# Kernel optimization log

Measured on AMD Instinct MI355X. Metric: run time of the kernel, lower is better.

## Reference

```python
import jax, jax.numpy as jnp
import numpy as np

V, H, B, T = 32000, 1024, 32, 256  # vocab, rnn_size, batch, seq_length


def setup_inputs() -> dict:
    key = jax.random.key(0)
    ks = jax.random.split(key, 6)
    s = 1.0 / np.sqrt(H)
    return {
        "input_data": jax.random.randint(ks[0], (B, T), 0, V, dtype=jnp.int32),
        "targets": jax.random.randint(ks[1], (B, T), 0, V, dtype=jnp.int32),
        "embedding": jax.random.uniform(ks[2], (V, H), minval=-1.0, maxval=1.0, dtype=jnp.float32),
        "softmax_b": jnp.zeros((V,), jnp.float32),
        "W0": (jax.random.normal(ks[3], (2 * H, 4 * H)) * s).astype(jnp.float32),
        "b0": jnp.zeros((4 * H,), jnp.float32),
        "W1": (jax.random.normal(ks[4], (2 * H, 4 * H)) * s).astype(jnp.float32),
        "b1": jnp.zeros((4 * H,), jnp.float32),
    }


def _lstm_step(x, c, h, W, b):
    # TF LSTMCell: gates i, j, f, o; forget_bias = 1.0
    z = jnp.concatenate([x, h], axis=-1) @ W + b  # [B, 4H]
    i, j, f, o = jnp.split(z, 4, axis=-1)
    c2 = c * jax.nn.sigmoid(f + 1.0) + jax.nn.sigmoid(i) * jnp.tanh(j)
    h2 = jax.nn.sigmoid(o) * jnp.tanh(c2)
    return c2, h2


def reference(input_data, targets, embedding, softmax_b, W0, b0, W1, b1):
    x = embedding[input_data]  # [B, T, H]
    Bb, Hh = x.shape[0], embedding.shape[1]
    zeros = jnp.zeros((Bb, Hh), x.dtype)
    init = ((zeros, zeros), (zeros, zeros))  # ((c0,h0),(c1,h1))

    def step(carry, xt):
        (c0, h0), (c1, h1) = carry
        c0, h0 = _lstm_step(xt, c0, h0, W0, b0)
        c1, h1 = _lstm_step(h0, c1, h1, W1, b1)
        return ((c0, h0), (c1, h1)), h1

    _, outs = jax.lax.scan(step, init, jnp.swapaxes(x, 0, 1))  # [T, B, H]
    output = jnp.swapaxes(outs, 0, 1).reshape(-1, Hh)  # [B*T, H]
    logits = output @ embedding.T + softmax_b  # tied softmax weights, [B*T, V]
    labels = targets.reshape(-1)
    logp = jax.nn.log_softmax(logits)
    loss = -jnp.take_along_axis(logp, labels[:, None], axis=1)[:, 0]
    cost = jnp.sum(loss) / Bb
    return logits, cost
```

## Files before the change

### kernel.cpp

```cpp
#include <hip/hip_runtime.h>
#include <hip/hip_bf16.h>

#define DEV static __device__ __forceinline__

typedef unsigned short u16;
typedef unsigned long long u64;
typedef __attribute__((ext_vector_type(8))) short short8;
typedef __attribute__((ext_vector_type(4))) float f32x4;

constexpr int V = 32000, H = 1024, B = 32, T = 256;
constexpr int BT = B * T;
constexpr int G  = 4 * H;
constexpr int NCH = V / 256;
constexpr int NWG2 = 256;
constexpr int RSTRIDE = 32 * 2048 + 2048;

constexpr size_t SZ_WT    = (size_t)G * 2048 * 2;
constexpr size_t OFF_W0T  = 0;
constexpr size_t OFF_W1T  = OFF_W0T + SZ_WT;
constexpr size_t OFF_EBF  = OFF_W1T + SZ_WT;
constexpr size_t OFF_XBF  = OFF_EBF + (size_t)V * H * 2;
constexpr size_t OFF_XP0  = OFF_XBF + (size_t)BT * H * 2;
constexpr size_t OFF_H1   = OFF_XP0 + (size_t)BT * G * 2;
constexpr size_t OFF_HSEQ = OFF_H1 + (size_t)BT * H * 2;
constexpr size_t SZ_HSEQ  = (size_t)(T + 2) * RSTRIDE * 2;
constexpr size_t OFF_SYNC = OFF_HSEQ + SZ_HSEQ;
constexpr size_t SZ_SYNC  = (size_t)2 * 256 * 128 * 4;
constexpr size_t OFF_PMAX = OFF_SYNC + SZ_SYNC;
constexpr size_t OFF_PSUM = OFF_PMAX + (size_t)BT * NCH * 4;
constexpr size_t OFF_LOSS = OFF_PSUM + (size_t)BT * NCH * 4;

DEV u16 f2bf(float x) {
  union { float f; unsigned int u; } v; v.f = x;
  unsigned int r = v.u + 0x7fffu + ((v.u >> 16) & 1u);
  return (u16)(r >> 16);
}
DEV float bf2f(u16 b) {
  union { unsigned int u; float f; } v; v.u = ((unsigned int)b) << 16;
  return v.f;
}
DEV float sigm(float x) { return 1.f / (1.f + expf(-x)); }

DEV void gload_lds16(const u16* g, u16* l) {
  __builtin_amdgcn_global_load_lds(
      (__attribute__((address_space(1))) void*)g,
      (__attribute__((address_space(3))) void*)l, 16, 0, 0);
}


__global__ void k_transpose_cvt(const float* __restrict__ in, u16* __restrict__ out,
                                int R, int C) {
  __shared__ float tile[32][33];
  int bc = blockIdx.x * 32, br = blockIdx.y * 32;
  int tx = threadIdx.x & 31, ty0 = threadIdx.x >> 5;
#pragma unroll
  for (int i = 0; i < 4; ++i) {
    int ty = ty0 + i * 8;
    tile[ty][tx] = in[(size_t)(br + ty) * C + bc + tx];
  }
  __syncthreads();
#pragma unroll
  for (int i = 0; i < 4; ++i) {
    int ty = ty0 + i * 8;
    out[(size_t)(bc + ty) * R + br + tx] = f2bf(tile[tx][ty]);
  }
}

__global__ void k_cvt_bf16(const float* __restrict__ in, u16* __restrict__ out, int n4) {
  int i = blockIdx.x * blockDim.x + threadIdx.x;
  int stride = gridDim.x * blockDim.x;
  for (; i < n4; i += stride) {
    float4 v = ((const float4*)in)[i];
    ushort4 o;
    o.x = f2bf(v.x); o.y = f2bf(v.y); o.z = f2bf(v.z); o.w = f2bf(v.w);
    ((ushort4*)out)[i] = o;
  }
}

__global__ void k_gather_x(const float* __restrict__ emb, const int* __restrict__ inp,
                           u16* __restrict__ Xbf) {
  int row = blockIdx.x;
  int t = row >> 5, b = row & 31;
  int tok = inp[b * T + t];
  const float4* src = (const float4*)(emb + (size_t)tok * H);
  ushort4* dst = (ushort4*)(Xbf + (size_t)row * H);
  float4 v = src[threadIdx.x];
  ushort4 o;
  o.x = f2bf(v.x); o.y = f2bf(v.y); o.z = f2bf(v.z); o.w = f2bf(v.w);
  dst[threadIdx.x] = o;
}

__global__ void k_zero(unsigned int* __restrict__ p, int nwords) {
  int i = blockIdx.x * blockDim.x + threadIdx.x;
  int stride = gridDim.x * blockDim.x;
  for (; i < nwords; i += stride) p[i] = 0u;
}

template <int CMODE>
__global__ __launch_bounds__(256)
void k_gemm(const u16* __restrict__ A, int lda,
            const u16* __restrict__ Bt, int ldb,
            float* __restrict__ C, int ldc,
            const float* __restrict__ bias, int K) {
  __shared__ alignas(16) u16 ldsA[128 * 32];
  __shared__ alignas(16) u16 ldsB[128 * 32];

  unsigned nwg = gridDim.x * gridDim.y;
  unsigned flat = blockIdx.y * gridDim.x + blockIdx.x;
  unsigned nf = (flat & 7) * (nwg >> 3) + (flat >> 3);
  unsigned bx = nf % gridDim.x, by = nf / gridDim.x;

  int tid = threadIdx.x, lane = tid & 63, w = tid >> 6;
  int row0 = by * 128, col0 = bx * 128;
  int wr = w >> 1, wc = w & 1;
  int c15 = lane & 15, q4 = lane >> 4;

  const u16* ag[2]; const u16* bg[2];
#pragma unroll
  for (int j = 0; j < 2; ++j) {
    int r = (j * 4 + w) * 16 + (lane >> 2);
    int k = (lane & 3) * 8;
    ag[j] = A + (size_t)(row0 + r) * lda + k;
    bg[j] = Bt + (size_t)(col0 + r) * ldb + k;
  }
  u16* lA0 = ldsA + (size_t)(0 + w) * 512;
  u16* lA1 = ldsA + (size_t)(4 + w) * 512;
  u16* lB0 = ldsB + (size_t)(0 + w) * 512;
  u16* lB1 = ldsB + (size_t)(4 + w) * 512;

  f32x4 acc[4][4];
#pragma unroll
  for (int m = 0; m < 4; ++m)
#pragma unroll
    for (int n = 0; n < 4; ++n) acc[m][n] = (f32x4){0.f, 0.f, 0.f, 0.f};

  int nk = K >> 5;
  for (int kk = 0; kk < nk; ++kk) {
    int kb = kk * 32;
    gload_lds16(ag[0] + kb, lA0);
    gload_lds16(ag[1] + kb, lA1);
    gload_lds16(bg[0] + kb, lB0);
    gload_lds16(bg[1] + kb, lB1);
    __syncthreads();

    short8 af[4], bfr[4];
#pragma unroll
    for (int m = 0; m < 4; ++m)
      af[m] = *(const short8*)(ldsA + (wr * 64 + m * 16 + c15) * 32 + q4 * 8);
#pragma unroll
    for (int n = 0; n < 4; ++n)
      bfr[n] = *(const short8*)(ldsB + (wc * 64 + n * 16 + c15) * 32 + q4 * 8);
#pragma unroll
    for (int m = 0; m < 4; ++m)
#pragma unroll
      for (int n = 0; n < 4; ++n)
        acc[m][n] = __builtin_amdgcn_mfma_f32_16x16x32_bf16(af[m], bfr[n], acc[m][n], 0, 0, 0);
    __syncthreads();
  }

  float bias_n[4];
#pragma unroll
  for (int n = 0; n < 4; ++n) bias_n[n] = bias[col0 + wc * 64 + n * 16 + c15];

#pragma unroll
  for (int m = 0; m < 4; ++m) {
#pragma unroll
    for (int jr = 0; jr < 4; ++jr) {
      int r_g = row0 + wr * 64 + m * 16 + q4 * 4 + jr;
#pragma unroll
      for (int n = 0; n < 4; ++n) {
        int c_g = col0 + wc * 64 + n * 16 + c15;
        float val = acc[m][n][jr] + bias_n[n];
        if (CMODE == 0) {
          C[(size_t)r_g * ldc + c_g] = val;
        } else {
          int tt = r_g >> 5, bb = r_g & 31;
          int q = c_g >> 10, wgup = (c_g & 1023) >> 3, uu = c_g & 7;
          ((u16*)C)[((((size_t)tt * 128 + wgup) * 32 + bb) * 32) + q * 8 + uu] = f2bf(val);
        }
      }
    }
  }
}

constexpr int GNT = 32;

DEV void stage_half256(const u16* __restrict__ A, int lda,
                       const u16* __restrict__ Bt, int ldb,
                       int row0, int col0, u16* lds, int Hh, int tid) {
  int t = Hh >> 2, j = Hh & 3, op = j >> 1, hh = j & 1;
  int wid = tid >> 6, lane = tid & 63;
  int r = hh * 128 + wid * 16 + (lane >> 2);
  int k = t * 32 + (((lane & 3) ^ ((lane >> 2) & 3)) << 3);
  const u16* g = (op == 0) ? (A + (size_t)(row0 + r) * lda + k)
                           : (Bt + (size_t)(col0 + r) * ldb + k);
  u16* l = lds + (size_t)((op * 2 + (t & 1)) * 8192 + (hh * 128 + wid * 16) * 32);
  gload_lds16(g, l);
}

template <bool SM_EPI>
__global__ __launch_bounds__(512)
void k_gemm256(const u16* __restrict__ A, int lda,
               const u16* __restrict__ Bt, int ldb,
               float* __restrict__ C, int ldc,
               const float* __restrict__ bias,
               float* __restrict__ pmax, float* __restrict__ psum, int nch) {
  __shared__ alignas(16) u16 lds[4 * 8192];

  unsigned nwg = gridDim.x * gridDim.y;
  unsigned flat = blockIdx.y * gridDim.x + blockIdx.x;
  unsigned nf = (flat & 7) * (nwg >> 3) + (flat >> 3);
  int bx = nf % gridDim.x, by = nf / gridDim.x;
  int row0 = by * 256, col0 = bx * 256;

  int tid = threadIdx.x, lane = tid & 63, wid = tid >> 6;
  int wr = wid >> 2, wc = wid & 3;
  int c15 = lane & 15, q4 = lane >> 4;
  int usw = (q4 ^ (c15 & 3)) << 3;

  f32x4 acc[8][4];
#pragma unroll
  for (int m = 0; m < 8; ++m)
#pragma unroll
    for (int n = 0; n < 4; ++n) acc[m][n] = (f32x4){0.f, 0.f, 0.f, 0.f};

#pragma unroll
  for (int h = 0; h < 7; ++h)
    stage_half256(A, lda, Bt, ldb, row0, col0, lds, h, tid);
  asm volatile("s_waitcnt vmcnt(3)" ::: "memory");
  __builtin_amdgcn_sched_barrier(0);
  __builtin_amdgcn_s_barrier();

  int Hh = 7;
  short8 af[4], bfr[4];

  for (int t = 0; t < GNT; ++t) {
    int pt = t & 1;
    const u16* la = lds + pt * 8192;
    const u16* lb = lds + (2 + pt) * 8192;

#pragma unroll
    for (int m = 0; m < 4; ++m)
      af[m] = *(const short8*)(la + (wr * 128 + m * 16 + c15) * 32 + usw);
#pragma unroll
    for (int n = 0; n < 4; ++n)
      bfr[n] = *(const short8*)(lb + (wc * 64 + n * 16 + c15) * 32 + usw);
    if (Hh < 4 * GNT) { stage_half256(A, lda, Bt, ldb, row0, col0, lds, Hh, tid); ++Hh; }
    if (Hh < 4 * GNT) { stage_half256(A, lda, Bt, ldb, row0, col0, lds, Hh, tid); ++Hh; }
    __builtin_amdgcn_s_barrier();
    asm volatile("s_waitcnt lgkmcnt(0)" ::: "memory");
    __builtin_amdgcn_sched_barrier(0);
    __builtin_amdgcn_s_setprio(1);
#pragma unroll
    for (int m = 0; m < 4; ++m)
#pragma unroll
      for (int n = 0; n < 4; ++n)
        acc[m][n] = __builtin_amdgcn_mfma_f32_16x16x32_bf16(af[m], bfr[n], acc[m][n], 0, 0, 0);
    __builtin_amdgcn_s_setprio(0);
    __builtin_amdgcn_s_barrier();

#pragma unroll
    for (int m = 0; m < 4; ++m)
      af[m] = *(const short8*)(la + (wr * 128 + (m + 4) * 16 + c15) * 32 + usw);
    if (Hh < 4 * GNT) { stage_half256(A, lda, Bt, ldb, row0, col0, lds, Hh, tid); ++Hh; }
    if (Hh < 4 * GNT) { stage_half256(A, lda, Bt, ldb, row0, col0, lds, Hh, tid); ++Hh; }
    __builtin_amdgcn_s_barrier();
    asm volatile("s_waitcnt lgkmcnt(0)" ::: "memory");
    __builtin_amdgcn_sched_barrier(0);
    __builtin_amdgcn_s_setprio(1);
#pragma unroll
    for (int m = 0; m < 4; ++m)
#pragma unroll
      for (int n = 0; n < 4; ++n)
        acc[m + 4][n] = __builtin_amdgcn_mfma_f32_16x16x32_bf16(af[m], bfr[n], acc[m + 4][n], 0, 0, 0);
    __builtin_amdgcn_s_setprio(0);
    if (t < GNT - 2) {
      asm volatile("s_waitcnt vmcnt(3)" ::: "memory");
      __builtin_amdgcn_sched_barrier(0);
    } else if (t == GNT - 2) {
      asm volatile("s_waitcnt vmcnt(0)" ::: "memory");
      __builtin_amdgcn_sched_barrier(0);
    }
    __builtin_amdgcn_s_barrier();
  }

  float bias_n[4];
#pragma unroll
  for (int n = 0; n < 4; ++n) bias_n[n] = bias[col0 + wc * 64 + n * 16 + c15];

  float2* red = (float2*)lds;
  __syncthreads();

#pragma unroll
  for (int m = 0; m < 8; ++m) {
#pragma unroll
    for (int jr = 0; jr < 4; ++jr) {
      int rloc = wr * 128 + m * 16 + q4 * 4 + jr;
      int r_g = row0 + rloc;
      float v[4];
#pragma unroll
      for (int n = 0; n < 4; ++n) {
        int c_g = col0 + wc * 64 + n * 16 + c15;
        float val = acc[m][n][jr] + bias_n[n];
        C[(size_t)r_g * ldc + c_g] = val;
        v[n] = val;
      }
      if (SM_EPI) {
        float mx = fmaxf(fmaxf(v[0], v[1]), fmaxf(v[2], v[3]));
        float s = __expf(v[0] - mx) + __expf(v[1] - mx) + __expf(v[2] - mx) + __expf(v[3] - mx);
#pragma unroll
        for (int d = 1; d < 16; d <<= 1) {
          float mo = __shfl_xor(mx, d, 64);
          float so = __shfl_xor(s, d, 64);
          float M2 = fmaxf(mx, mo);
          s = s * __expf(mx - M2) + so * __expf(mo - M2);
          mx = M2;
        }
        if (c15 == 0) red[rloc * 4 + wc] = make_float2(mx, s);
      }
    }
  }
  if (SM_EPI) {
    __syncthreads();
    if (tid < 256) {
      float M = -1e30f, S = 0.f;
#pragma unroll
      for (int i = 0; i < 4; ++i) {
        float2 a = red[tid * 4 + i];
        float M2 = fmaxf(M, a.x);
        S = S * __expf(M - M2) + a.y * __expf(a.x - M2);
        M = M2;
      }
      pmax[(size_t)(row0 + tid) * nch + bx] = M;
      psum[(size_t)(row0 + tid) * nch + bx] = S;
    }
  }
}


#define RED(w_, bt_, nt_, r_, c_) red[((((w_)*2 + (bt_)) * 2 + (nt_)) * 16 + (r_)) * 16 + (c_)]

DEV void wait_flags(const int* __restrict__ fa, const int* __restrict__ fb) {
  if (threadIdx.x < 64) {
    int lane = threadIdx.x;
    while (true) {
      int ok = 1;
      if (fa) {
        int a0 = __hip_atomic_load(fa + lane,      __ATOMIC_RELAXED, __HIP_MEMORY_SCOPE_AGENT);
        int a1 = __hip_atomic_load(fa + 64 + lane, __ATOMIC_RELAXED, __HIP_MEMORY_SCOPE_AGENT);
        ok &= (a0 != 0) & (a1 != 0);
      }
      if (fb) {
        int b0 = __hip_atomic_load(fb + lane,      __ATOMIC_RELAXED, __HIP_MEMORY_SCOPE_AGENT);
        int b1 = __hip_atomic_load(fb + 64 + lane, __ATOMIC_RELAXED, __HIP_MEMORY_SCOPE_AGENT);
        ok &= (b0 != 0) & (b1 != 0);
      }
      if (__all(ok)) break;
      __builtin_amdgcn_s_sleep(1);
    }
  }
  __builtin_amdgcn_sched_barrier(0);
  __syncthreads();
}

DEV void publish_flag(int* __restrict__ word) {
  __syncthreads();
  if (threadIdx.x == 0)
    __hip_atomic_store(word, 1, __ATOMIC_RELAXED, __HIP_MEMORY_SCOPE_AGENT);
}

template <int KH, bool IS_L0>
DEV void lstm_role(const u16* __restrict__ WT,
                   const u16* __restrict__ xp0p,
                   const float* __restrict__ zb1,
                   u16* __restrict__ hseq, u16* __restrict__ H1bf,
                   int* __restrict__ f0, int* __restrict__ f1,
                   float* __restrict__ red, int wgu) {
  constexpr int KOFF = IS_L0 ? 1024 : 0;
  constexpr int KS = KH / 4;
  constexpr int NKC = KS / 32;
  int tid = threadIdx.x, lane = tid & 63, w = tid >> 6;
  int c15 = lane & 15, q4 = lane >> 4;
  int eb = tid >> 3, eu = tid & 7;

  short8 wfr[2][NKC];
#pragma unroll
  for (int nt = 0; nt < 2; ++nt) {
    int lr = nt * 16 + c15;
    const u16* rp = WT + (size_t)((lr >> 3) * 1024 + wgu * 8 + (lr & 7)) * 2048
                    + KOFF + w * KS + q4 * 8;
#pragma unroll
    for (int kc = 0; kc < NKC; ++kc)
      wfr[nt][kc] = *(const short8*)(rp + kc * 32);
  }

  float zpc[4];
  if (!IS_L0) {
#pragma unroll
    for (int q = 0; q < 4; ++q) zpc[q] = zb1[q * 1024 + wgu * 8 + eu];
  }
  float creg = 0.f;

  for (int it_t = 0; it_t < T; ++it_t) {
    int t = IS_L0 ? it_t : it_t + 1;

    float zp[4];
    if (IS_L0) {
#pragma unroll
      for (int q = 0; q < 4; ++q)
        zp[q] = bf2f(xp0p[((((size_t)t * 128 + wgu) * 32 + eb) * 32) + q * 8 + eu]);
    } else {
#pragma unroll
      for (int q = 0; q < 4; ++q) zp[q] = zpc[q];
    }

    if (IS_L0) {
      if (t >= 1) wait_flags(f0 + (size_t)(t - 1) * 128, nullptr);
    } else {
      wait_flags(f0 + (size_t)(t - 1) * 128,
                 t >= 2 ? f1 + (size_t)(t - 2) * 128 : nullptr);
    }

    const u16* hread = hseq + (size_t)t * RSTRIDE;
    f32x4 acc[2][2];
#pragma unroll
    for (int bt = 0; bt < 2; ++bt)
#pragma unroll
      for (int nt = 0; nt < 2; ++nt) acc[bt][nt] = (f32x4){0.f, 0.f, 0.f, 0.f};

#pragma unroll
    for (int kc = 0; kc < NKC; ++kc) {
      int kh = w * KS + kc * 32 + q4 * 8;
      short8 a0 = *(const short8*)(hread + (size_t)c15 * 2048 + kh);
      short8 a1 = *(const short8*)(hread + (size_t)(16 + c15) * 2048 + kh);
      acc[0][0] = __builtin_amdgcn_mfma_f32_16x16x32_bf16(a0, wfr[0][kc], acc[0][0], 0, 0, 0);
      acc[0][1] = __builtin_amdgcn_mfma_f32_16x16x32_bf16(a0, wfr[1][kc], acc[0][1], 0, 0, 0);
      acc[1][0] = __builtin_amdgcn_mfma_f32_16x16x32_bf16(a1, wfr[0][kc], acc[1][0], 0, 0, 0);
      acc[1][1] = __builtin_amdgcn_mfma_f32_16x16x32_bf16(a1, wfr[1][kc], acc[1][1], 0, 0, 0);
    }

#pragma unroll
    for (int bt = 0; bt < 2; ++bt)
#pragma unroll
      for (int nt = 0; nt < 2; ++nt)
#pragma unroll
        for (int jr = 0; jr < 4; ++jr)
          RED(w, bt, nt, q4 * 4 + jr, c15) = acc[bt][nt][jr];
    __syncthreads();

    int bt = eb >> 4, rr = eb & 15;
    float z[4];
#pragma unroll
    for (int q = 0; q < 4; ++q) {
      int lr = q * 8 + eu, nt = lr >> 4, cc = lr & 15;
      z[q] = RED(0, bt, nt, rr, cc) + RED(1, bt, nt, rr, cc) +
             RED(2, bt, nt, rr, cc) + RED(3, bt, nt, rr, cc) + zp[q];
    }
    float gi = sigm(z[0]);
    float gj = tanhf(z[1]);
    float gf = sigm(z[2] + 1.f);
    float go = sigm(z[3]);
    creg = creg * gf + gi * gj;
    float hv = go * tanhf(creg);

    int hb = (int)f2bf(hv);
    int hp = __shfl_xor(hb, 1, 64);
    if (!(tid & 1)) {
      unsigned int pack = (unsigned int)(u16)hb | ((unsigned int)(u16)hp << 16);
      u16* hwr = hseq + (size_t)(t + 1) * RSTRIDE + (IS_L0 ? 0 : 1024);
      __hip_atomic_store((unsigned int*)(hwr + (size_t)eb * 2048 + wgu * 8 + eu), pack,
                         __ATOMIC_RELAXED, __HIP_MEMORY_SCOPE_AGENT);
      if (!IS_L0)
        __builtin_nontemporal_store(pack,
            (unsigned int*)(H1bf + ((size_t)eb * T + (t - 1)) * H + wgu * 8 + eu));
    }

    publish_flag(IS_L0 ? (f0 + (size_t)t * 128 + wgu)
                       : (f1 + (size_t)(t - 1) * 128 + wgu));
  }
}

__global__ __launch_bounds__(256, 1)
void k_lstm_persistent(const u16* __restrict__ W0T, const u16* __restrict__ W1T,
                       const u16* __restrict__ xp0p, const float* __restrict__ b1,
                       u16* __restrict__ hseq, u16* __restrict__ H1bf,
                       int* __restrict__ sync) {
  __shared__ float red[4 * 2 * 2 * 16 * 16];
  int* f0 = sync;
  int* f1 = sync + 256 * 128;
  int wg = blockIdx.x;
  if (wg < 128)
    lstm_role<1024, true>(W0T, xp0p, nullptr, hseq, H1bf, f0, f1, red, wg);
  else
    lstm_role<2048, false>(W1T, nullptr, b1, hseq, H1bf, f0, f1, red, wg - 128);
}

__global__ void k_rowfin(const float* __restrict__ pmax, const float* __restrict__ psum,
                         const float* __restrict__ Cl, const int* __restrict__ targets,
                         float* __restrict__ loss) {
  int row = blockIdx.x;
  int tid = threadIdx.x, lane = tid & 63, w = tid >> 6;
  float mx = -1e30f, s = 0.f;
  if (tid < NCH) { mx = pmax[(size_t)row * NCH + tid]; s = psum[(size_t)row * NCH + tid]; }
#pragma unroll
  for (int d = 1; d < 64; d <<= 1) {
    float mo = __shfl_xor(mx, d, 64);
    float so = __shfl_xor(s, d, 64);
    float M2 = fmaxf(mx, mo);
    s = s * __expf(mx - M2) + so * __expf(mo - M2);
    mx = M2;
  }
  __shared__ float2 wred[4];
  if (lane == 0) wred[w] = make_float2(mx, s);
  __syncthreads();
  if (tid == 0) {
    float M = wred[0].x, S = wred[0].y;
#pragma unroll
    for (int i = 1; i < 4; ++i) {
      float M2 = fmaxf(M, wred[i].x);
      S = S * __expf(M - M2) + wred[i].y * __expf(wred[i].x - M2);
      M = M2;
    }
    float logZ = M + logf(S);
    int tgt = targets[row];
    float xt = Cl[(size_t)row * V + tgt];
    loss[row] = logZ - xt;
  }
}

__global__ void k_cost(const float* __restrict__ loss, float* __restrict__ out) {
  int tid = threadIdx.x, lane = tid & 63, w = tid >> 6;
  float s = 0.f;
  for (int i = tid; i < BT; i += 256) s += loss[i];
#pragma unroll
  for (int d = 1; d < 64; d <<= 1) s += __shfl_xor(s, d, 64);
  __shared__ float ws4[4];
  if (lane == 0) ws4[w] = s;
  __syncthreads();
  if (tid == 0) out[0] = (ws4[0] + ws4[1] + ws4[2] + ws4[3]) * (1.0f / B);
}

extern "C" void kernel_launch(void* const* d_in, const int* in_sizes, int n_in,
                              void* d_out, int out_size, void* d_ws, size_t ws_size,
                              hipStream_t stream) {
  const int*   input_data = (const int*)d_in[0];
  const int*   targets    = (const int*)d_in[1];
  const float* emb        = (const float*)d_in[2];
  const float* softmax_b  = (const float*)d_in[3];
  const float* W0         = (const float*)d_in[4];
  const float* b0         = (const float*)d_in[5];
  const float* W1         = (const float*)d_in[6];
  const float* b1         = (const float*)d_in[7];
  float* out = (float*)d_out;
  char*  ws  = (char*)d_ws;

  u16*   W0T  = (u16*)(ws + OFF_W0T);
  u16*   W1T  = (u16*)(ws + OFF_W1T);
  u16*   Ebf  = (u16*)(ws + OFF_EBF);
  u16*   Xbf  = (u16*)(ws + OFF_XBF);
  u16*   xp0p = (u16*)(ws + OFF_XP0);
  u16*   H1bf = (u16*)(ws + OFF_H1);
  u16*   hseq = (u16*)(ws + OFF_HSEQ);
  int*   sync = (int*)(ws + OFF_SYNC);
  float* pmax = (float*)(ws + OFF_PMAX);
  float* psum = (float*)(ws + OFF_PSUM);
  float* lossb= (float*)(ws + OFF_LOSS);

  k_transpose_cvt<<<dim3(G / 32, 2048 / 32), 256, 0, stream>>>(W0, W0T, 2048, G);
  k_transpose_cvt<<<dim3(G / 32, 2048 / 32), 256, 0, stream>>>(W1, W1T, 2048, G);
  k_cvt_bf16<<<2048, 256, 0, stream>>>(emb, Ebf, V * H / 4);
  k_gather_x<<<BT, 256, 0, stream>>>(emb, input_data, Xbf);
  k_zero<<<64, 256, 0, stream>>>((unsigned int*)(ws + OFF_HSEQ), RSTRIDE);
  k_zero<<<64, 256, 0, stream>>>((unsigned int*)(ws + OFF_SYNC), (int)(SZ_SYNC / 4));

  k_gemm<1><<<dim3(G / 128, BT / 128), 256, 0, stream>>>(
      Xbf, H, W0T, 2048, (float*)xp0p, G, b0, H);

  k_lstm_persistent<<<dim3(NWG2), dim3(256), 0, stream>>>(
      W0T, W1T, xp0p, b1, hseq, H1bf, sync);

  k_gemm256<true><<<dim3(V / 256, BT / 256), 512, 0, stream>>>(
      H1bf, H, Ebf, H, out, V, softmax_b, pmax, psum, NCH);

  k_rowfin<<<BT, 256, 0, stream>>>(pmax, psum, out, targets, lossb);
  k_cost<<<1, 256, 0, stream>>>(lossb, out + (size_t)BT * V);
}
```

Before: 2.991 ms.

## Restructure persistent LSTM into 96 wide blocks and triple-buffer logits GEMM

The persistent LSTM kernel changes from 256 blocks of 256 threads, which reduced partial sums across waves through LDS, to 96 blocks of 512 threads. Layer 0 gets 32 blocks in which each wave owns 4 units over the full K, so no cross-wave reduction is needed. Layer 1 gets 64 blocks that split K in two halves. Sync flags are padded to separate cache lines, the h operands are software-prefetched in registers, and the xp0 layout is reordered to match the new unit mapping. Separately, the vocab GEMM moves from a double-buffered to a triple-buffered LDS pipeline, staging tile t+2. Fewer blocks per timestep should cut flag-polling and barrier cost, but each block does more serial MFMA work and holds a large register working set.

New measurement: 5.297 ms. 1.77x slower.

```diff
diff --git a/kernel.cpp b/kernel.cpp
--- a/kernel.cpp
+++ b/kernel.cpp
@@ -12,7 +12,8 @@
 constexpr int BT = B * T;
 constexpr int G  = 4 * H;
 constexpr int NCH = V / 256;
-constexpr int NWG2 = 256;
+constexpr int NWG3 = 96;
+constexpr int FSTR = 16;
 constexpr int RSTRIDE = 32 * 2048 + 2048;
 
 constexpr size_t SZ_WT    = (size_t)G * 2048 * 2;
@@ -25,7 +26,7 @@
 constexpr size_t OFF_HSEQ = OFF_H1 + (size_t)BT * H * 2;
 constexpr size_t SZ_HSEQ  = (size_t)(T + 2) * RSTRIDE * 2;
 constexpr size_t OFF_SYNC = OFF_HSEQ + SZ_HSEQ;
-constexpr size_t SZ_SYNC  = (size_t)2 * 256 * 128 * 4;
+constexpr size_t SZ_SYNC  = (size_t)(256 * 32 + 256 * 64) * FSTR * 4;
 constexpr size_t OFF_PMAX = OFF_SYNC + SZ_SYNC;
 constexpr size_t OFF_PSUM = OFF_PMAX + (size_t)BT * NCH * 4;
 constexpr size_t OFF_LOSS = OFF_PSUM + (size_t)BT * NCH * 4;
@@ -175,8 +176,10 @@
           C[(size_t)r_g * ldc + c_g] = val;
         } else {
           int tt = r_g >> 5, bb = r_g & 31;
-          int q = c_g >> 10, wgup = (c_g & 1023) >> 3, uu = c_g & 7;
-          ((u16*)C)[((((size_t)tt * 128 + wgup) * 32 + bb) * 32) + q * 8 + uu] = f2bf(val);
+          int q = c_g >> 10, U = c_g & 1023;
+          int ub = U >> 5, wvi = (U >> 2) & 7, uu = U & 3;
+          ((u16*)C)[(((((size_t)tt * 32 + ub) * 8 + wvi) * 16 + q * 4 + uu) * 32) + bb]
+              = f2bf(val);
         }
       }
     }
@@ -185,16 +188,16 @@
 
 constexpr int GNT = 32;
 
-DEV void stage_half256(const u16* __restrict__ A, int lda,
-                       const u16* __restrict__ Bt, int ldb,
-                       int row0, int col0, u16* lds, int Hh, int tid) {
-  int t = Hh >> 2, j = Hh & 3, op = j >> 1, hh = j & 1;
+DEV void stage256(const u16* __restrict__ A, int lda,
+                  const u16* __restrict__ Bt, int ldb,
+                  int row0, int col0, u16* lds, int t, int h, int tid) {
+  int op = h >> 1, hh = h & 1;
   int wid = tid >> 6, lane = tid & 63;
   int r = hh * 128 + wid * 16 + (lane >> 2);
   int k = t * 32 + (((lane & 3) ^ ((lane >> 2) & 3)) << 3);
   const u16* g = (op == 0) ? (A + (size_t)(row0 + r) * lda + k)
                            : (Bt + (size_t)(col0 + r) * ldb + k);
-  u16* l = lds + (size_t)((op * 2 + (t & 1)) * 8192 + (hh * 128 + wid * 16) * 32);
+  u16* l = lds + (size_t)((op * 3 + (t % 3)) * 8192 + (hh * 128 + wid * 16) * 32);
   gload_lds16(g, l);
 }
 
@@ -205,7 +208,7 @@
                float* __restrict__ C, int ldc,
                const float* __restrict__ bias,
                float* __restrict__ pmax, float* __restrict__ psum, int nch) {
-  __shared__ alignas(16) u16 lds[4 * 8192];
+  __shared__ alignas(16) u16 lds[6 * 8192];
 
   unsigned nwg = gridDim.x * gridDim.y;
   unsigned flat = blockIdx.y * gridDim.x + blockIdx.x;
@@ -225,19 +228,18 @@
     for (int n = 0; n < 4; ++n) acc[m][n] = (f32x4){0.f, 0.f, 0.f, 0.f};
 
 #pragma unroll
-  for (int h = 0; h < 7; ++h)
-    stage_half256(A, lda, Bt, ldb, row0, col0, lds, h, tid);
-  asm volatile("s_waitcnt vmcnt(3)" ::: "memory");
+  for (int h = 0; h < 4; ++h) stage256(A, lda, Bt, ldb, row0, col0, lds, 0, h, tid);
+#pragma unroll
+  for (int h = 0; h < 4; ++h) stage256(A, lda, Bt, ldb, row0, col0, lds, 1, h, tid);
+  asm volatile("s_waitcnt vmcnt(4)" ::: "memory");
   __builtin_amdgcn_sched_barrier(0);
   __builtin_amdgcn_s_barrier();
 
-  int Hh = 7;
   short8 af[4], bfr[4];
 
   for (int t = 0; t < GNT; ++t) {
-    int pt = t & 1;
-    const u16* la = lds + pt * 8192;
-    const u16* lb = lds + (2 + pt) * 8192;
+    const u16* la = lds + (size_t)(t % 3) * 8192;
+    const u16* lb = lds + (size_t)(3 + t % 3) * 8192;
 
 #pragma unroll
     for (int m = 0; m < 4; ++m)
@@ -245,8 +247,10 @@
 #pragma unroll
     for (int n = 0; n < 4; ++n)
       bfr[n] = *(const short8*)(lb + (wc * 64 + n * 16 + c15) * 32 + usw);
-    if (Hh < 4 * GNT) { stage_half256(A, lda, Bt, ldb, row0, col0, lds, Hh, tid); ++Hh; }
-    if (Hh < 4 * GNT) { stage_half256(A, lda, Bt, ldb, row0, col0, lds, Hh, tid); ++Hh; }
+    if (t + 2 < GNT) {
+      stage256(A, lda, Bt, ldb, row0, col0, lds, t + 2, 0, tid);
+      stage256(A, lda, Bt, ldb, row0, col0, lds, t + 2, 1, tid);
+    }
     __builtin_amdgcn_s_barrier();
     asm volatile("s_waitcnt lgkmcnt(0)" ::: "memory");
     __builtin_amdgcn_sched_barrier(0);
@@ -262,8 +266,10 @@
 #pragma unroll
     for (int m = 0; m < 4; ++m)
       af[m] = *(const short8*)(la + (wr * 128 + (m + 4) * 16 + c15) * 32 + usw);
-    if (Hh < 4 * GNT) { stage_half256(A, lda, Bt, ldb, row0, col0, lds, Hh, tid); ++Hh; }
-    if (Hh < 4 * GNT) { stage_half256(A, lda, Bt, ldb, row0, col0, lds, Hh, tid); ++Hh; }
+    if (t + 2 < GNT) {
+      stage256(A, lda, Bt, ldb, row0, col0, lds, t + 2, 2, tid);
+      stage256(A, lda, Bt, ldb, row0, col0, lds, t + 2, 3, tid);
+    }
     __builtin_amdgcn_s_barrier();
     asm volatile("s_waitcnt lgkmcnt(0)" ::: "memory");
     __builtin_amdgcn_sched_barrier(0);
@@ -275,7 +281,7 @@
         acc[m + 4][n] = __builtin_amdgcn_mfma_f32_16x16x32_bf16(af[m], bfr[n], acc[m + 4][n], 0, 0, 0);
     __builtin_amdgcn_s_setprio(0);
     if (t < GNT - 2) {
-      asm volatile("s_waitcnt vmcnt(3)" ::: "memory");
+      asm volatile("s_waitcnt vmcnt(4)" ::: "memory");
       __builtin_amdgcn_sched_barrier(0);
     } else if (t == GNT - 2) {
       asm volatile("s_waitcnt vmcnt(0)" ::: "memory");
@@ -338,161 +344,202 @@
 }
 
 
-#define RED(w_, bt_, nt_, r_, c_) red[((((w_)*2 + (bt_)) * 2 + (nt_)) * 16 + (r_)) * 16 + (c_)]
-
-DEV void wait_flags(const int* __restrict__ fa, const int* __restrict__ fb) {
-  if (threadIdx.x < 64) {
-    int lane = threadIdx.x;
-    while (true) {
-      int ok = 1;
-      if (fa) {
-        int a0 = __hip_atomic_load(fa + lane,      __ATOMIC_RELAXED, __HIP_MEMORY_SCOPE_AGENT);
-        int a1 = __hip_atomic_load(fa + 64 + lane, __ATOMIC_RELAXED, __HIP_MEMORY_SCOPE_AGENT);
-        ok &= (a0 != 0) & (a1 != 0);
-      }
-      if (fb) {
-        int b0 = __hip_atomic_load(fb + lane,      __ATOMIC_RELAXED, __HIP_MEMORY_SCOPE_AGENT);
-        int b1 = __hip_atomic_load(fb + 64 + lane, __ATOMIC_RELAXED, __HIP_MEMORY_SCOPE_AGENT);
-        ok &= (b0 != 0) & (b1 != 0);
-      }
-      if (__all(ok)) break;
-      __builtin_amdgcn_s_sleep(1);
-    }
-  }
-  __builtin_amdgcn_sched_barrier(0);
-  __syncthreads();
-}
-
-DEV void publish_flag(int* __restrict__ word) {
-  __syncthreads();
-  if (threadIdx.x == 0)
-    __hip_atomic_store(word, 1, __ATOMIC_RELAXED, __HIP_MEMORY_SCOPE_AGENT);
-}
-
-template <int KH, bool IS_L0>
-DEV void lstm_role(const u16* __restrict__ WT,
-                   const u16* __restrict__ xp0p,
-                   const float* __restrict__ zb1,
-                   u16* __restrict__ hseq, u16* __restrict__ H1bf,
-                   int* __restrict__ f0, int* __restrict__ f1,
-                   float* __restrict__ red, int wgu) {
-  constexpr int KOFF = IS_L0 ? 1024 : 0;
-  constexpr int KS = KH / 4;
-  constexpr int NKC = KS / 32;
-  int tid = threadIdx.x, lane = tid & 63, w = tid >> 6;
+DEV int flag_ld(const int* p) {
+  return __hip_atomic_load(p, __ATOMIC_RELAXED, __HIP_MEMORY_SCOPE_AGENT);
+}
+
+DEV void wave_poll(const int* fa, int na, const int* fb) {
+  int lane = threadIdx.x & 63;
+  while (true) {
+    int ok = 1;
+    if (lane < na) ok = (flag_ld(fa + (size_t)lane * FSTR) != 0);
+    if (fb) ok &= (flag_ld(fb + (size_t)lane * FSTR) != 0);
+    if (__all(ok)) break;
+    __builtin_amdgcn_s_sleep(1);
+  }
+}
+
+__global__ __launch_bounds__(512, 2)
+void k_lstm2(const u16* __restrict__ W0T, const u16* __restrict__ W1T,
+             const u16* __restrict__ xp0p, const float* __restrict__ b1,
+             u16* __restrict__ hseq, u16* __restrict__ H1bf,
+             int* __restrict__ sync) {
+  __shared__ float zlds[8][2][16][16];
+  int wg = blockIdx.x;
+  int tid = threadIdx.x, lane = tid & 63, wv = tid >> 6;
   int c15 = lane & 15, q4 = lane >> 4;
-  int eb = tid >> 3, eu = tid & 7;
-
-  short8 wfr[2][NKC];
-#pragma unroll
-  for (int nt = 0; nt < 2; ++nt) {
-    int lr = nt * 16 + c15;
-    const u16* rp = WT + (size_t)((lr >> 3) * 1024 + wgu * 8 + (lr & 7)) * 2048
-                    + KOFF + w * KS + q4 * 8;
-#pragma unroll
-    for (int kc = 0; kc < NKC; ++kc)
-      wfr[nt][kc] = *(const short8*)(rp + kc * 32);
-  }
-
-  float zpc[4];
-  if (!IS_L0) {
-#pragma unroll
-    for (int q = 0; q < 4; ++q) zpc[q] = zb1[q * 1024 + wgu * 8 + eu];
-  }
-  float creg = 0.f;
-
-  for (int it_t = 0; it_t < T; ++it_t) {
-    int t = IS_L0 ? it_t : it_t + 1;
-
-    float zp[4];
-    if (IS_L0) {
-#pragma unroll
-      for (int q = 0; q < 4; ++q)
-        zp[q] = bf2f(xp0p[((((size_t)t * 128 + wgu) * 32 + eb) * 32) + q * 8 + eu]);
-    } else {
-#pragma unroll
-      for (int q = 0; q < 4; ++q) zp[q] = zpc[q];
-    }
-
-    if (IS_L0) {
-      if (t >= 1) wait_flags(f0 + (size_t)(t - 1) * 128, nullptr);
-    } else {
-      wait_flags(f0 + (size_t)(t - 1) * 128,
-                 t >= 2 ? f1 + (size_t)(t - 2) * 128 : nullptr);
-    }
-
-    const u16* hread = hseq + (size_t)t * RSTRIDE;
-    f32x4 acc[2][2];
-#pragma unroll
-    for (int bt = 0; bt < 2; ++bt)
-#pragma unroll
-      for (int nt = 0; nt < 2; ++nt) acc[bt][nt] = (f32x4){0.f, 0.f, 0.f, 0.f};
-
-#pragma unroll
-    for (int kc = 0; kc < NKC; ++kc) {
-      int kh = w * KS + kc * 32 + q4 * 8;
-      short8 a0 = *(const short8*)(hread + (size_t)c15 * 2048 + kh);
-      short8 a1 = *(const short8*)(hread + (size_t)(16 + c15) * 2048 + kh);
-      acc[0][0] = __builtin_amdgcn_mfma_f32_16x16x32_bf16(a0, wfr[0][kc], acc[0][0], 0, 0, 0);
-      acc[0][1] = __builtin_amdgcn_mfma_f32_16x16x32_bf16(a0, wfr[1][kc], acc[0][1], 0, 0, 0);
-      acc[1][0] = __builtin_amdgcn_mfma_f32_16x16x32_bf16(a1, wfr[0][kc], acc[1][0], 0, 0, 0);
-      acc[1][1] = __builtin_amdgcn_mfma_f32_16x16x32_bf16(a1, wfr[1][kc], acc[1][1], 0, 0, 0);
-    }
-
-#pragma unroll
-    for (int bt = 0; bt < 2; ++bt)
-#pragma unroll
-      for (int nt = 0; nt < 2; ++nt)
-#pragma unroll
-        for (int jr = 0; jr < 4; ++jr)
-          RED(w, bt, nt, q4 * 4 + jr, c15) = acc[bt][nt][jr];
-    __syncthreads();
-
-    int bt = eb >> 4, rr = eb & 15;
-    float z[4];
-#pragma unroll
-    for (int q = 0; q < 4; ++q) {
-      int lr = q * 8 + eu, nt = lr >> 4, cc = lr & 15;
-      z[q] = RED(0, bt, nt, rr, cc) + RED(1, bt, nt, rr, cc) +
-             RED(2, bt, nt, rr, cc) + RED(3, bt, nt, rr, cc) + zp[q];
-    }
-    float gi = sigm(z[0]);
-    float gj = tanhf(z[1]);
-    float gf = sigm(z[2] + 1.f);
-    float go = sigm(z[3]);
-    creg = creg * gf + gi * gj;
-    float hv = go * tanhf(creg);
-
-    int hb = (int)f2bf(hv);
-    int hp = __shfl_xor(hb, 1, 64);
-    if (!(tid & 1)) {
-      unsigned int pack = (unsigned int)(u16)hb | ((unsigned int)(u16)hp << 16);
-      u16* hwr = hseq + (size_t)(t + 1) * RSTRIDE + (IS_L0 ? 0 : 1024);
-      __hip_atomic_store((unsigned int*)(hwr + (size_t)eb * 2048 + wgu * 8 + eu), pack,
-                         __ATOMIC_RELAXED, __HIP_MEMORY_SCOPE_AGENT);
-      if (!IS_L0)
-        __builtin_nontemporal_store(pack,
-            (unsigned int*)(H1bf + ((size_t)eb * T + (t - 1)) * H + wgu * 8 + eu));
-    }
-
-    publish_flag(IS_L0 ? (f0 + (size_t)t * 128 + wgu)
-                       : (f1 + (size_t)(t - 1) * 128 + wgu));
-  }
-}
-
-__global__ __launch_bounds__(256, 1)
-void k_lstm_persistent(const u16* __restrict__ W0T, const u16* __restrict__ W1T,
-                       const u16* __restrict__ xp0p, const float* __restrict__ b1,
-                       u16* __restrict__ hseq, u16* __restrict__ H1bf,
-                       int* __restrict__ sync) {
-  __shared__ float red[4 * 2 * 2 * 16 * 16];
+  int u = lane & 3, b0e = lane >> 2;
   int* f0 = sync;
-  int* f1 = sync + 256 * 128;
-  int wg = blockIdx.x;
-  if (wg < 128)
-    lstm_role<1024, true>(W0T, xp0p, nullptr, hseq, H1bf, f0, f1, red, wg);
-  else
-    lstm_role<2048, false>(W1T, nullptr, b1, hseq, H1bf, f0, f1, red, wg - 128);
+  int* f1 = sync + (size_t)256 * 32 * FSTR;
+
+  if (wg < 32) {
+    int ub = wg;
+    int U0 = ub * 32 + wv * 4;
+    short8 wfr[32];
+    {
+      int q = c15 >> 2, u4 = c15 & 3;
+      const u16* rp = W0T + (size_t)(q * 1024 + U0 + u4) * 2048 + 1024 + q4 * 8;
+#pragma unroll
+      for (int ks = 0; ks < 32; ++ks) wfr[ks] = *(const short8*)(rp + ks * 32);
+    }
+    float cr0 = 0.f, cr1 = 0.f;
+
+    for (int t = 0; t < T; ++t) {
+      const u16* xb = xp0p + ((((size_t)t * 32 + ub) * 8 + wv) * 16) * 32;
+      u16 zpb0[4], zpb1[4];
+#pragma unroll
+      for (int q = 0; q < 4; ++q) {
+        zpb0[q] = xb[(q * 4 + u) * 32 + b0e];
+        zpb1[q] = xb[(q * 4 + u) * 32 + b0e + 16];
+      }
+      if (t >= 1) wave_poll(f0 + (size_t)(t - 1) * 32 * FSTR, 32, nullptr);
+
+      const u16* hread = hseq + (size_t)t * RSTRIDE;
+      f32x4 acc0 = (f32x4){0.f, 0.f, 0.f, 0.f}, acc1 = (f32x4){0.f, 0.f, 0.f, 0.f};
+      short8 af0[8], af1[8];
+#pragma unroll
+      for (int p = 0; p < 8; ++p) {
+        af0[p] = *(const short8*)(hread + (size_t)c15 * 2048 + p * 32 + q4 * 8);
+        af1[p] = *(const short8*)(hread + (size_t)(16 + c15) * 2048 + p * 32 + q4 * 8);
+      }
+#pragma unroll
+      for (int ks = 0; ks < 32; ++ks) {
+        int s = ks & 7;
+        short8 a0 = af0[s], a1 = af1[s];
+        if (ks < 24) {
+          af0[s] = *(const short8*)(hread + (size_t)c15 * 2048 + (ks + 8) * 32 + q4 * 8);
+          af1[s] = *(const short8*)(hread + (size_t)(16 + c15) * 2048 + (ks + 8) * 32 + q4 * 8);
+        }
+        acc0 = __builtin_amdgcn_mfma_f32_16x16x32_bf16(a0, wfr[ks], acc0, 0, 0, 0);
+        acc1 = __builtin_amdgcn_mfma_f32_16x16x32_bf16(a1, wfr[ks], acc1, 0, 0, 0);
+      }
+#pragma unroll
+      for (int j = 0; j < 4; ++j) {
+        zlds[wv][0][q4 * 4 + j][c15] = acc0[j];
+        zlds[wv][1][q4 * 4 + j][c15] = acc1[j];
+      }
+      float hv0, hv1;
+      {
+        float z[4];
+#pragma unroll
+        for (int q = 0; q < 4; ++q)
+          z[q] = zlds[wv][b0e >> 4][b0e & 15][q * 4 + u] + bf2f(zpb0[q]);
+        float gi = sigm(z[0]), gj = tanhf(z[1]), gf = sigm(z[2] + 1.f), go = sigm(z[3]);
+        cr0 = cr0 * gf + gi * gj;
+        hv0 = go * tanhf(cr0);
+      }
+      {
+        float z[4];
+#pragma unroll
+        for (int q = 0; q < 4; ++q)
+          z[q] = zlds[wv][1][b0e & 15][q * 4 + u] + bf2f(zpb1[q]);
+        float gi = sigm(z[0]), gj = tanhf(z[1]), gf = sigm(z[2] + 1.f), go = sigm(z[3]);
+        cr1 = cr1 * gf + gi * gj;
+        hv1 = go * tanhf(cr1);
+      }
+      int hb0 = (int)f2bf(hv0), hb1 = (int)f2bf(hv1);
+      int hp0 = __shfl_xor(hb0, 1, 64), hp1 = __shfl_xor(hb1, 1, 64);
+      if (!(lane & 1)) {
+        u16* hwr = hseq + (size_t)(t + 1) * RSTRIDE;
+        unsigned pk0 = (u16)hb0 | ((unsigned)(u16)hp0 << 16);
+        unsigned pk1 = (u16)hb1 | ((unsigned)(u16)hp1 << 16);
+        __hip_atomic_store((unsigned*)(hwr + (size_t)b0e * 2048 + U0 + u), pk0,
+                           __ATOMIC_RELAXED, __HIP_MEMORY_SCOPE_AGENT);
+        __hip_atomic_store((unsigned*)(hwr + (size_t)(b0e + 16) * 2048 + U0 + u), pk1,
+                           __ATOMIC_RELAXED, __HIP_MEMORY_SCOPE_AGENT);
+      }
+      __syncthreads();
+      if (tid == 0)
+        __hip_atomic_store(f0 + ((size_t)t * 32 + ub) * FSTR, 1,
+                           __ATOMIC_RELAXED, __HIP_MEMORY_SCOPE_AGENT);
+    }
+  } else {
+    int ub = wg - 32;
+    int grp = wv & 3, khalf = wv >> 2;
+    int U0 = ub * 16 + grp * 4;
+    short8 wfr[32];
+    {
+      int q = c15 >> 2, u4 = c15 & 3;
+      const u16* rp = W1T + (size_t)(q * 1024 + U0 + u4) * 2048 + khalf * 1024 + q4 * 8;
+#pragma unroll
+      for (int ks = 0; ks < 32; ++ks) wfr[ks] = *(const short8*)(rp + ks * 32);
+    }
+    float zpc[4];
+#pragma unroll
+    for (int q = 0; q < 4; ++q) zpc[q] = b1[q * 1024 + U0 + u];
+    float cr0 = 0.f, cr1 = 0.f;
+
+    for (int t = 1; t <= T; ++t) {
+      wave_poll(f0 + (size_t)(t - 1) * 32 * FSTR, 32,
+                t >= 2 ? f1 + (size_t)(t - 2) * 64 * FSTR : nullptr);
+
+      const u16* hread = hseq + (size_t)t * RSTRIDE + khalf * 1024;
+      f32x4 acc0 = (f32x4){0.f, 0.f, 0.f, 0.f}, acc1 = (f32x4){0.f, 0.f, 0.f, 0.f};
+      short8 af0[8], af1[8];
+#pragma unroll
+      for (int p = 0; p < 8; ++p) {
+        af0[p] = *(const short8*)(hread + (size_t)c15 * 2048 + p * 32 + q4 * 8);
+        af1[p] = *(const short8*)(hread + (size_t)(16 + c15) * 2048 + p * 32 + q4 * 8);
+      }
+#pragma unroll
+      for (int ks = 0; ks < 32; ++ks) {
+        int s = ks & 7;
+        short8 a0 = af0[s], a1 = af1[s];
+        if (ks < 24) {
+          af0[s] = *(const short8*)(hread + (size_t)c15 * 2048 + (ks + 8) * 32 + q4 * 8);
+          af1[s] = *(const short8*)(hread + (size_t)(16 + c15) * 2048 + (ks + 8) * 32 + q4 * 8);
+        }
+        acc0 = __builtin_amdgcn_mfma_f32_16x16x32_bf16(a0, wfr[ks], acc0, 0, 0, 0);
+        acc1 = __builtin_amdgcn_mfma_f32_16x16x32_bf16(a1, wfr[ks], acc1, 0, 0, 0);
+      }
+#pragma unroll
+      for (int j = 0; j < 4; ++j) {
+        zlds[grp * 2 + khalf][0][q4 * 4 + j][c15] = acc0[j];
+        zlds[grp * 2 + khalf][1][q4 * 4 + j][c15] = acc1[j];
+      }
+      __syncthreads();
+      if (khalf == 0) {
+        float hv0, hv1;
+        {
+          float z[4];
+#pragma unroll
+          for (int q = 0; q < 4; ++q)
+            z[q] = zlds[grp * 2][b0e >> 4][b0e & 15][q * 4 + u] +
+                   zlds[grp * 2 + 1][b0e >> 4][b0e & 15][q * 4 + u] + zpc[q];
+          float gi = sigm(z[0]), gj = tanhf(z[1]), gf = sigm(z[2] + 1.f), go = sigm(z[3]);
+          cr0 = cr0 * gf + gi * gj;
+          hv0 = go * tanhf(cr0);
+        }
+        {
+          float z[4];
+#pragma unroll
+          for (int q = 0; q < 4; ++q)
+            z[q] = zlds[grp * 2][1][b0e & 15][q * 4 + u] +
+                   zlds[grp * 2 + 1][1][b0e & 15][q * 4 + u] + zpc[q];
+          float gi = sigm(z[0]), gj = tanhf(z[1]), gf = sigm(z[2] + 1.f), go = sigm(z[3]);
+          cr1 = cr1 * gf + gi * gj;
+          hv1 = go * tanhf(cr1);
+        }
+        int hb0 = (int)f2bf(hv0), hb1 = (int)f2bf(hv1);
+        int hp0 = __shfl_xor(hb0, 1, 64), hp1 = __shfl_xor(hb1, 1, 64);
+        if (!(lane & 1)) {
+          u16* hwr = hseq + (size_t)(t + 1) * RSTRIDE + 1024;
+          unsigned pk0 = (u16)hb0 | ((unsigned)(u16)hp0 << 16);
+          unsigned pk1 = (u16)hb1 | ((unsigned)(u16)hp1 << 16);
+          __hip_atomic_store((unsigned*)(hwr + (size_t)b0e * 2048 + U0 + u), pk0,
+                             __ATOMIC_RELAXED, __HIP_MEMORY_SCOPE_AGENT);
+          __hip_atomic_store((unsigned*)(hwr + (size_t)(b0e + 16) * 2048 + U0 + u), pk1,
+                             __ATOMIC_RELAXED, __HIP_MEMORY_SCOPE_AGENT);
+          *(unsigned*)(H1bf + ((size_t)b0e * T + (t - 1)) * H + U0 + u) = pk0;
+          *(unsigned*)(H1bf + ((size_t)(b0e + 16) * T + (t - 1)) * H + U0 + u) = pk1;
+        }
+      }
+      __syncthreads();
+      if (tid == 0)
+        __hip_atomic_store(f1 + ((size_t)(t - 1) * 64 + ub) * FSTR, 1,
+                           __ATOMIC_RELAXED, __HIP_MEMORY_SCOPE_AGENT);
+    }
+  }
 }
 
 __global__ void k_rowfin(const float* __restrict__ pmax, const float* __restrict__ psum,
@@ -571,12 +618,12 @@
   k_cvt_bf16<<<2048, 256, 0, stream>>>(emb, Ebf, V * H / 4);
   k_gather_x<<<BT, 256, 0, stream>>>(emb, input_data, Xbf);
   k_zero<<<64, 256, 0, stream>>>((unsigned int*)(ws + OFF_HSEQ), RSTRIDE);
-  k_zero<<<64, 256, 0, stream>>>((unsigned int*)(ws + OFF_SYNC), (int)(SZ_SYNC / 4));
+  k_zero<<<256, 256, 0, stream>>>((unsigned int*)(ws + OFF_SYNC), (int)(SZ_SYNC / 4));
 
   k_gemm<1><<<dim3(G / 128, BT / 128), 256, 0, stream>>>(
       Xbf, H, W0T, 2048, (float*)xp0p, G, b0, H);
 
-  k_lstm_persistent<<<dim3(NWG2), dim3(256), 0, stream>>>(
+  k_lstm2<<<dim3(NWG3), dim3(512), 0, stream>>>(
       W0T, W1T, xp0p, b1, hseq, H1bf, sync);
 
   k_gemm256<true><<<dim3(V / 256, BT / 256), 512, 0, stream>>>(
```
